# Kernel optimization log

Measured on AMD Instinct MI355X. Metric: run time of the kernel, lower is better.

## Reference

```python
import jax, jax.numpy as jnp
import numpy as np

N = 100000
E = 3200000
FEAT_DIMS = [512, 256, 128]
NUM_GNN = 2
NUM_MLP = 2
EPS = 1e-12


def l2norm(x):
    # F.normalize(x, dim=1, p=2)
    n = jnp.sqrt(jnp.sum(x * x, axis=1, keepdims=True))
    return x / jnp.maximum(n, EPS)


def setup_inputs() -> dict:
    key = jax.random.key(0)
    ks = jax.random.split(key, 16)
    D = FEAT_DIMS[-1]
    inp = {
        "feat": jax.random.normal(ks[0], (N, FEAT_DIMS[0]), dtype=jnp.float32),
        "sup_rows": jax.random.randint(ks[1], (E,), 0, N, dtype=jnp.int32),
        "sup_cols": jax.random.randint(ks[2], (E,), 0, N, dtype=jnp.int32),
        "sup_vals": jax.random.uniform(ks[3], (E,), dtype=jnp.float32),
        # feature-reduction linears (stored [in, out])
        "W_feat0": jax.random.normal(ks[4], (FEAT_DIMS[0], FEAT_DIMS[1]), dtype=jnp.float32) * 0.05,
        "b_feat0": jnp.zeros((FEAT_DIMS[1],), dtype=jnp.float32),
        "W_feat1": jax.random.normal(ks[5], (FEAT_DIMS[1], FEAT_DIMS[2]), dtype=jnp.float32) * 0.05,
        "b_feat1": jnp.zeros((FEAT_DIMS[2],), dtype=jnp.float32),
        # GCN layers (bias=False)
        "W_gnn": jax.random.normal(ks[6], (NUM_GNN, D, D), dtype=jnp.float32) * 0.05,
        # final emb linear map
        "W_emb": jax.random.normal(ks[7], (D, D), dtype=jnp.float32) * 0.05,
        "b_emb": jnp.zeros((D,), dtype=jnp.float32),
        # temperature MLP towers
        "W_lft": jax.random.normal(ks[8], (NUM_MLP, D, D), dtype=jnp.float32) * 0.05,
        "b_lft": jnp.zeros((NUM_MLP, D), dtype=jnp.float32),
        "W_rgt": jax.random.normal(ks[9], (NUM_MLP, D, D), dtype=jnp.float32) * 0.05,
        "b_rgt": jnp.zeros((NUM_MLP, D), dtype=jnp.float32),
    }
    return inp


def _forward(feat, sup_rows, sup_cols, sup_vals,
             W_feat0, b_feat0, W_feat1, b_feat1,
             W_gnn, W_emb, b_emb, W_lft, b_lft, W_rgt, b_rgt):
    # non-linear feature reduction (dropout = identity in eval mode)
    x = jnp.tanh(feat @ W_feat0 + b_feat0)
    x = jnp.tanh(x @ W_feat1 + b_feat1)

    def spmm(emb):
        # sparse support @ emb via gather + segment-sum
        msgs = sup_vals[:, None] * emb[sup_cols]           # [E, D]
        return jax.ops.segment_sum(msgs, sup_rows, num_segments=N)

    gnn_in = x
    gnn_acc = x
    gnn_out = x
    for l in range(NUM_GNN):
        h = spmm(gnn_in)
        h = jnp.tanh(h @ W_gnn[l])
        gnn_out = l2norm(h)
        gnn_in = gnn_out
        gnn_acc = gnn_acc + gnn_out

    emb = l2norm(gnn_acc @ W_emb + b_emb)

    lft_in = gnn_out
    rgt_in = gnn_out
    for l in range(NUM_MLP):
        lft = jnp.tanh(lft_in @ W_lft[l] + b_lft[l])
        rgt = jnp.tanh(rgt_in @ W_rgt[l] + b_rgt[l])
        if l < NUM_MLP - 1:
            lft = lft + lft_in
            rgt = rgt + rgt_in
        lft_in, rgt_in = lft, rgt
    return emb, lft_in, rgt_in


def reference(feat, sup_rows, sup_cols, sup_vals,
              W_feat0, b_feat0, W_feat1, b_feat1,
              W_gnn, W_emb, b_emb, W_lft, b_lft, W_rgt, b_rgt):
    return _forward(feat, sup_rows, sup_cols, sup_vals,
                    W_feat0, b_feat0, W_feat1, b_feat1,
                    W_gnn, W_emb, b_emb, W_lft, b_lft, W_rgt, b_rgt)
```

## Files before the change

kernel.cpp:

```cpp
#include <hip/hip_runtime.h>
#include <math.h>

typedef short bf16x8 __attribute__((ext_vector_type(8)));
typedef float f32x4  __attribute__((ext_vector_type(4)));

__device__ __forceinline__ unsigned short f2bf(float x) {
    unsigned u = __float_as_uint(x);
    unsigned r = u + 0x7FFFu + ((u >> 16) & 1u);
    return (unsigned short)(r >> 16);
}
__device__ __forceinline__ float bf2f(unsigned short b) {
    return __uint_as_float(((unsigned)b) << 16);
}

__global__ __launch_bounds__(256)
void wconvD(const float* __restrict__ W, unsigned short* __restrict__ Wt, int K, int N)
{
    int id = blockIdx.x * 256 + threadIdx.x;
    if (id >= K * N) return;
    int c = id / K, k = id - c * K;
    int kblk = k >> 5, ksub = (k >> 3) & 3, kel = k & 7;
    int cblk = c >> 6, n = c & 3, lr = (c >> 2) & 15;
    int lane = lr + (ksub << 4);
    size_t dst = ((((size_t)kblk * (N >> 6) + cblk) * 4 + n) << 9) + (lane << 3) + kel;
    Wt[dst] = f2bf(W[(size_t)k * N + c]);
}

__global__ __launch_bounds__(256)
void wconv7(const float* __restrict__ Wg, const float* __restrict__ Wemb,
            const float* __restrict__ Wl, const float* __restrict__ Wr,
            unsigned short* __restrict__ dst)
{
    int id = blockIdx.x * 256 + threadIdx.x;
    if (id >= 7 * 16384) return;
    int m = id >> 14, r = id & 16383;
    int c = r >> 7, k = r & 127;
    const float* src = (m < 2) ? (Wg + m * 16384)
                     : (m == 2) ? Wemb
                     : (m < 5) ? (Wl + (m - 3) * 16384)
                               : (Wr + (m - 5) * 16384);
    int n = c & 7, lr = (c >> 3) & 15;
    int ks = k >> 5, ksub = (k >> 3) & 3, kel = k & 7;
    int lane = lr + (ksub << 4);
    dst[(size_t)m * 16384 + (((ks << 3) + n) << 9) + (lane << 3) + kel] = f2bf(src[(size_t)k * 128 + c]);
}

__global__ __launch_bounds__(256)
void f32_to_bf16(const float* __restrict__ in, unsigned short* __restrict__ outb, long n8)
{
    long id = (long)blockIdx.x * 256 + threadIdx.x;
    if (id >= n8) return;
    const float4* p = (const float4*)(in + id * 8);
    float4 a = p[0], b = p[1];
    *(ushort4*)(outb + id * 8)     = make_ushort4(f2bf(a.x), f2bf(a.y), f2bf(a.z), f2bf(a.w));
    *(ushort4*)(outb + id * 8 + 4) = make_ushort4(f2bf(b.x), f2bf(b.y), f2bf(b.z), f2bf(b.w));
}

__global__ __launch_bounds__(512)
void mfma_head(const unsigned short* __restrict__ Ab, const unsigned short* __restrict__ Wt0,
               const float* __restrict__ bf0, const unsigned short* __restrict__ Wt1,
               const float* __restrict__ bf1, unsigned short* __restrict__ x_bf, int M)
{
    __shared__ __align__(16) unsigned short x1s[4][16][264];

    const int tid  = threadIdx.x;
    const int wv   = tid >> 6, lane = tid & 63;
    const int rg   = wv >> 1, ch = wv & 1;
    const int lr   = lane & 15;
    const int lk8  = (lane >> 4) * 8;
    const int rbase = (lane >> 4) * 4;
    const int row0 = blockIdx.x * 64 + rg * 16;

    const unsigned short* arow;
    { int r = row0 + lr; r = r < M ? r : (M - 1); arow = Ab + (size_t)r * 512 + lk8; }
    const unsigned short* bb0 = Wt0 + ((((size_t)ch * 2) * 4) << 9) + (lane << 3);

    f32x4 acc1[8];
#pragma unroll
    for (int s = 0; s < 8; s++)
#pragma unroll
        for (int q = 0; q < 4; q++) acc1[s][q] = 0.f;

#pragma unroll 2
    for (int kb = 0; kb < 16; kb++) {
        bf16x8 af = *(const bf16x8*)(arow + kb * 32);
        bf16x8 bn[8];
        const unsigned short* bk = bb0 + (((size_t)kb * 16) << 9);
#pragma unroll
        for (int s = 0; s < 8; s++) bn[s] = *(const bf16x8*)(bk + ((size_t)s << 9));
#pragma unroll
        for (int s = 0; s < 8; s++)
            acc1[s] = __builtin_amdgcn_mfma_f32_16x16x32_bf16(af, bn[s], acc1[s], 0, 0, 0);
    }

#pragma unroll
    for (int cb = 0; cb < 2; cb++) {
        int colp = (ch * 2 + cb) * 64 + lr * 4;
        float4 b4 = *(const float4*)(bf0 + colp);
        float bv[4] = {b4.x, b4.y, b4.z, b4.w};
#pragma unroll
        for (int j = 0; j < 4; j++) {
            ushort4 o;
            o.x = f2bf(tanhf(acc1[cb * 4 + 0][j] + bv[0]));
            o.y = f2bf(tanhf(acc1[cb * 4 + 1][j] + bv[1]));
            o.z = f2bf(tanhf(acc1[cb * 4 + 2][j] + bv[2]));
            o.w = f2bf(tanhf(acc1[cb * 4 + 3][j] + bv[3]));
            *(ushort4*)&x1s[rg][rbase + j][colp] = o;
        }
    }
    __syncthreads();

    const unsigned short* bb1 = Wt1 + ((((size_t)ch) * 4) << 9) + (lane << 3);

    f32x4 acc2[4];
#pragma unroll
    for (int n = 0; n < 4; n++)
#pragma unroll
        for (int q = 0; q < 4; q++) acc2[n][q] = 0.f;

#pragma unroll 2
    for (int ks = 0; ks < 8; ks++) {
        bf16x8 af = *(const bf16x8*)&x1s[rg][lr][ks * 32 + lk8];
        bf16x8 bn[4];
        const unsigned short* bk = bb1 + (((size_t)ks * 8) << 9);
#pragma unroll
        for (int n = 0; n < 4; n++) bn[n] = *(const bf16x8*)(bk + ((size_t)n << 9));
#pragma unroll
        for (int n = 0; n < 4; n++)
            acc2[n] = __builtin_amdgcn_mfma_f32_16x16x32_bf16(af, bn[n], acc2[n], 0, 0, 0);
    }

    const int cbase = ch * 64 + lr * 4;
    float4 b4 = *(const float4*)(bf1 + cbase);
    float bv[4] = {b4.x, b4.y, b4.z, b4.w};
#pragma unroll
    for (int j = 0; j < 4; j++) {
        int row = row0 + rbase + j;
        if (row < M) {
            ushort4 o;
            o.x = f2bf(tanhf(acc2[0][j] + bv[0]));
            o.y = f2bf(tanhf(acc2[1][j] + bv[1]));
            o.z = f2bf(tanhf(acc2[2][j] + bv[2]));
            o.w = f2bf(tanhf(acc2[3][j] + bv[3]));
            *(ushort4*)(x_bf + ((size_t)row << 7) + cbase) = o;
        }
    }
}

template<bool ABF16, bool TANH, bool L2, bool RESID, bool AUX, bool AUXBF,
         bool F32OUT, bool BF16OUT, bool BIAS>
__global__ __launch_bounds__(256)
void mfma_ep(const void* __restrict__ A_, const unsigned short* __restrict__ Wt,
             const float* __restrict__ bias, const unsigned short* __restrict__ resid_bf,
             const void* __restrict__ aux_in, float* __restrict__ aux_out,
             float* __restrict__ out, unsigned short* __restrict__ out_bf, int M)
{
    const int tid  = threadIdx.x;
    const int row0 = blockIdx.x * 64;
    const int wv   = tid >> 6, lane = tid & 63;
    const int lr   = lane & 15;
    const int lk8  = (lane >> 4) * 8;
    const int wr   = wv * 16;

    const unsigned short* Abr;
    const float*          Afr;
    {
        int r = row0 + wr + lr;
        r = r < M ? r : (M - 1);
        Abr = (const unsigned short*)A_ + ((size_t)r << 7) + lk8;
        Afr = (const float*)A_          + ((size_t)r << 7) + lk8;
    }
    const unsigned short* wb = Wt + (lane << 3);

    f32x4 acc[8];
#pragma unroll
    for (int n = 0; n < 8; n++)
#pragma unroll
        for (int j = 0; j < 4; j++) acc[n][j] = 0.f;

#pragma unroll 2
    for (int ks = 0; ks < 4; ks++) {
        bf16x8 af, bn[8];
        if (ABF16) af = *(const bf16x8*)(Abr + ks * 32);
        else {
            float4 a = *(const float4*)(Afr + ks * 32);
            float4 b = *(const float4*)(Afr + ks * 32 + 4);
            af[0]=(short)f2bf(a.x); af[1]=(short)f2bf(a.y); af[2]=(short)f2bf(a.z); af[3]=(short)f2bf(a.w);
            af[4]=(short)f2bf(b.x); af[5]=(short)f2bf(b.y); af[6]=(short)f2bf(b.z); af[7]=(short)f2bf(b.w);
        }
#pragma unroll
        for (int n = 0; n < 8; n++)
            bn[n] = *(const bf16x8*)(wb + ((((ks << 3) + n)) << 9));
#pragma unroll
        for (int n = 0; n < 8; n++)
            acc[n] = __builtin_amdgcn_mfma_f32_16x16x32_bf16(af, bn[n], acc[n], 0, 0, 0);
    }

    const int cbase = lr * 8;
    float bv[8];
    if (BIAS) {
        float4 b0 = *(const float4*)(bias + cbase);
        float4 b1 = *(const float4*)(bias + cbase + 4);
        bv[0]=b0.x; bv[1]=b0.y; bv[2]=b0.z; bv[3]=b0.w;
        bv[4]=b1.x; bv[5]=b1.y; bv[6]=b1.z; bv[7]=b1.w;
    } else {
#pragma unroll
        for (int n = 0; n < 8; n++) bv[n] = 0.f;
    }
    const int rbase = (lane >> 4) * 4;

#pragma unroll
    for (int j = 0; j < 4; j++) {
        int row = row0 + wr + rbase + j;
        bool ok = row < M;
        size_t base = ((size_t)row << 7) + cbase;
        float v[8];
#pragma unroll
        for (int n = 0; n < 8; n++) {
            v[n] = acc[n][j] + bv[n];
            if (TANH) v[n] = tanhf(v[n]);
        }
        if (RESID) {
            if (ok) {
                bf16x8 rv = *(const bf16x8*)(resid_bf + base);
#pragma unroll
                for (int n = 0; n < 8; n++) v[n] += bf2f((unsigned short)rv[n]);
            }
        }
        if (L2) {
            float s = 0.f;
#pragma unroll
            for (int n = 0; n < 8; n++) s += v[n] * v[n];
#pragma unroll
            for (int msk = 8; msk >= 1; msk >>= 1) s += __shfl_xor(s, msk);
            float sc = 1.f / fmaxf(sqrtf(s), 1e-12f);
#pragma unroll
            for (int n = 0; n < 8; n++) v[n] *= sc;
        }
        if (ok) {
            if (F32OUT) {
                *(float4*)(out + base)     = make_float4(v[0], v[1], v[2], v[3]);
                *(float4*)(out + base + 4) = make_float4(v[4], v[5], v[6], v[7]);
            }
            if (BF16OUT) {
                bf16x8 o;
#pragma unroll
                for (int n = 0; n < 8; n++) o[n] = (short)f2bf(v[n]);
                *(bf16x8*)(out_bf + base) = o;
            }
            if (AUX) {
                float ai[8];
                if (AUXBF) {
                    bf16x8 av = *(const bf16x8*)((const unsigned short*)aux_in + base);
#pragma unroll
                    for (int n = 0; n < 8; n++) ai[n] = bf2f((unsigned short)av[n]);
                } else {
                    float4 a0 = *(const float4*)((const float*)aux_in + base);
                    float4 a1 = *(const float4*)((const float*)aux_in + base + 4);
                    ai[0]=a0.x; ai[1]=a0.y; ai[2]=a0.z; ai[3]=a0.w;
                    ai[4]=a1.x; ai[5]=a1.y; ai[6]=a1.z; ai[7]=a1.w;
                }
                *(float4*)(aux_out + base)     = make_float4(ai[0]+v[0], ai[1]+v[1], ai[2]+v[2], ai[3]+v[3]);
                *(float4*)(aux_out + base + 4) = make_float4(ai[4]+v[4], ai[5]+v[5], ai[6]+v[6], ai[7]+v[7]);
            }
        }
    }
}

__global__ __launch_bounds__(256)
void tail_fused(const unsigned short* __restrict__ h_bf, const float* __restrict__ accf,
                const unsigned short* __restrict__ Wt7,
                const float* __restrict__ bemb, const float* __restrict__ bl,
                const float* __restrict__ br,
                float* __restrict__ embO, float* __restrict__ lftO,
                float* __restrict__ rgtO, int M)
{
    __shared__ __align__(16) unsigned short ldsA[4][16][136];
    __shared__ __align__(16) unsigned short ldsB[4][16][136];

    const int tid = threadIdx.x;
    const int wv = tid >> 6, lane = tid & 63;
    const int lr = lane & 15;
    const int lk8 = (lane >> 4) * 8;
    const int rbase = (lane >> 4) * 4;
    const int row0 = blockIdx.x * 64 + wv * 16;
    const int cbase = lr * 8;

    const unsigned short* Wg1t  = Wt7 + 1 * 16384 + (lane << 3);
    const unsigned short* Wembt = Wt7 + 2 * 16384 + (lane << 3);
    const unsigned short* Wl0t  = Wt7 + 3 * 16384 + (lane << 3);
    const unsigned short* Wl1t  = Wt7 + 4 * 16384 + (lane << 3);
    const unsigned short* Wr0t  = Wt7 + 5 * 16384 + (lane << 3);
    const unsigned short* Wr1t  = Wt7 + 6 * 16384 + (lane << 3);

    f32x4 acc[8];

#define ZACC() { _Pragma("unroll") for (int n = 0; n < 8; n++) \
                 _Pragma("unroll") for (int q = 0; q < 4; q++) acc[n][q] = 0.f; }
#define MM128(AFRAG, WPTR)                                                            \
    _Pragma("unroll")                                                                 \
    for (int ks = 0; ks < 4; ks++) {                                                  \
        bf16x8 af = (AFRAG);                                                          \
        bf16x8 bn[8];                                                                 \
        _Pragma("unroll")                                                             \
        for (int n = 0; n < 8; n++)                                                   \
            bn[n] = *(const bf16x8*)((WPTR) + ((((ks << 3) + n)) << 9));              \
        _Pragma("unroll")                                                             \
        for (int n = 0; n < 8; n++)                                                   \
            acc[n] = __builtin_amdgcn_mfma_f32_16x16x32_bf16(af, bn[n], acc[n], 0, 0, 0); \
    }
#define LDBIAS(BV, P) { float4 b0_ = *(const float4*)((P) + cbase);                   \
                        float4 b1_ = *(const float4*)((P) + cbase + 4);               \
                        BV[0]=b0_.x; BV[1]=b0_.y; BV[2]=b0_.z; BV[3]=b0_.w;           \
                        BV[4]=b1_.x; BV[5]=b1_.y; BV[6]=b1_.z; BV[7]=b1_.w; }
#define L2NORM(V) { float s_ = 0.f;                                                   \
                    _Pragma("unroll") for (int n = 0; n < 8; n++) s_ += V[n]*V[n];    \
                    _Pragma("unroll") for (int mk = 8; mk >= 1; mk >>= 1) s_ += __shfl_xor(s_, mk); \
                    float sc_ = 1.f / fmaxf(sqrtf(s_), 1e-12f);                       \
                    _Pragma("unroll") for (int n = 0; n < 8; n++) V[n] *= sc_; }

    const unsigned short* hrow;
    {
        int r = row0 + lr;
        r = r < M ? r : (M - 1);
        hrow = h_bf + ((size_t)r << 7) + lk8;
    }
    ZACC();
    MM128(*(const bf16x8*)(hrow + ks * 32), Wg1t);
#pragma unroll
    for (int j = 0; j < 4; j++) {
        int row = row0 + rbase + j;
        int rc = row < M ? row : (M - 1);
        float v[8];
#pragma unroll
        for (int n = 0; n < 8; n++) v[n] = tanhf(acc[n][j]);
        L2NORM(v);
        bf16x8 o;
#pragma unroll
        for (int n = 0; n < 8; n++) o[n] = (short)f2bf(v[n]);
        *(bf16x8*)&ldsA[wv][rbase + j][cbase] = o;
        float4 a0 = *(const float4*)(accf + ((size_t)rc << 7) + cbase);
        float4 a1 = *(const float4*)(accf + ((size_t)rc << 7) + cbase + 4);
        float av[8] = {a0.x+v[0], a0.y+v[1], a0.z+v[2], a0.w+v[3],
                       a1.x+v[4], a1.y+v[5], a1.z+v[6], a1.w+v[7]};
        bf16x8 ob;
#pragma unroll
        for (int n = 0; n < 8; n++) ob[n] = (short)f2bf(av[n]);
        *(bf16x8*)&ldsB[wv][rbase + j][cbase] = ob;
    }

    ZACC();
    MM128(*(const bf16x8*)&ldsB[wv][lr][ks * 32 + lk8], Wembt);
    {
        float bv[8]; LDBIAS(bv, bemb);
#pragma unroll
        for (int j = 0; j < 4; j++) {
            int row = row0 + rbase + j;
            float v[8];
#pragma unroll
            for (int n = 0; n < 8; n++) v[n] = acc[n][j] + bv[n];
            L2NORM(v);
            if (row < M) {
                size_t base = ((size_t)row << 7) + cbase;
                *(float4*)(embO + base)     = make_float4(v[0], v[1], v[2], v[3]);
                *(float4*)(embO + base + 4) = make_float4(v[4], v[5], v[6], v[7]);
            }
        }
    }

    ZACC();
    MM128(*(const bf16x8*)&ldsA[wv][lr][ks * 32 + lk8], Wl0t);
    {
        float bv[8]; LDBIAS(bv, bl);
#pragma unroll
        for (int j = 0; j < 4; j++) {
            bf16x8 rv = *(const bf16x8*)&ldsA[wv][rbase + j][cbase];
            bf16x8 ob;
#pragma unroll
            for (int n = 0; n < 8; n++)
                ob[n] = (short)f2bf(tanhf(acc[n][j] + bv[n]) + bf2f((unsigned short)rv[n]));
            *(bf16x8*)&ldsB[wv][rbase + j][cbase] = ob;
        }
    }

    ZACC();
    MM128(*(const bf16x8*)&ldsB[wv][lr][ks * 32 + lk8], Wl1t);
    {
        float bv[8]; LDBIAS(bv, bl + 128);
#pragma unroll
        for (int j = 0; j < 4; j++) {
            int row = row0 + rbase + j;
            if (row < M) {
                size_t base = ((size_t)row << 7) + cbase;
                *(float4*)(lftO + base)     = make_float4(tanhf(acc[0][j]+bv[0]), tanhf(acc[1][j]+bv[1]),
                                                          tanhf(acc[2][j]+bv[2]), tanhf(acc[3][j]+bv[3]));
                *(float4*)(lftO + base + 4) = make_float4(tanhf(acc[4][j]+bv[4]), tanhf(acc[5][j]+bv[5]),
                                                          tanhf(acc[6][j]+bv[6]), tanhf(acc[7][j]+bv[7]));
            }
        }
    }

    ZACC();
    MM128(*(const bf16x8*)&ldsA[wv][lr][ks * 32 + lk8], Wr0t);
    {
        float bv[8]; LDBIAS(bv, br);
#pragma unroll
        for (int j = 0; j < 4; j++) {
            bf16x8 rv = *(const bf16x8*)&ldsA[wv][rbase + j][cbase];
            bf16x8 ob;
#pragma unroll
            for (int n = 0; n < 8; n++)
                ob[n] = (short)f2bf(tanhf(acc[n][j] + bv[n]) + bf2f((unsigned short)rv[n]));
            *(bf16x8*)&ldsB[wv][rbase + j][cbase] = ob;
        }
    }

    ZACC();
    MM128(*(const bf16x8*)&ldsB[wv][lr][ks * 32 + lk8], Wr1t);
    {
        float bv[8]; LDBIAS(bv, br + 128);
#pragma unroll
        for (int j = 0; j < 4; j++) {
            int row = row0 + rbase + j;
            if (row < M) {
                size_t base = ((size_t)row << 7) + cbase;
                *(float4*)(rgtO + base)     = make_float4(tanhf(acc[0][j]+bv[0]), tanhf(acc[1][j]+bv[1]),
                                                          tanhf(acc[2][j]+bv[2]), tanhf(acc[3][j]+bv[3]));
                *(float4*)(rgtO + base + 4) = make_float4(tanhf(acc[4][j]+bv[4]), tanhf(acc[5][j]+bv[5]),
                                                          tanhf(acc[6][j]+bv[6]), tanhf(acc[7][j]+bv[7]));
            }
        }
    }
#undef ZACC
#undef MM128
#undef LDBIAS
#undef L2NORM
}

#define RCHUNK 16384

__global__ __launch_bounds__(256)
void bhist_k(const int* __restrict__ rows, int* __restrict__ bcnt, int E, int NB)
{
    __shared__ int lc[1024];
    for (int b = threadIdx.x; b < NB; b += 256) lc[b] = 0;
    __syncthreads();
    int start = blockIdx.x * RCHUNK;
    int end = min(start + RCHUNK, E);
    for (int i = start + threadIdx.x; i < end; i += 256)
        atomicAdd(&lc[rows[i] >> 7], 1);
    __syncthreads();
    for (int b = threadIdx.x; b < NB; b += 256)
        if (lc[b]) atomicAdd(&bcnt[b], lc[b]);
}

__global__ __launch_bounds__(256)
void bucket_scan(const int* __restrict__ bcnt, int* __restrict__ bbase,
                 int* __restrict__ bcur, int NB)
{
    __shared__ int sdata[256];
    const int tid = threadIdx.x;
    int loc[4]; int s = 0;
#pragma unroll
    for (int j = 0; j < 4; j++) {
        int i = tid * 4 + j;
        int v = (i < NB) ? bcnt[i] : 0;
        loc[j] = s; s += v;
    }
    sdata[tid] = s;
    __syncthreads();
    int x = s;
    for (int off = 1; off < 256; off <<= 1) {
        int t = 0;
        if (tid >= off) t = sdata[tid - off];
        __syncthreads();
        x += t;
        sdata[tid] = x;
        __syncthreads();
    }
    int excl = x - s;
#pragma unroll
    for (int j = 0; j < 4; j++) {
        int i = tid * 4 + j;
        if (i < NB) { bbase[i] = excl + loc[j]; bcur[i] = excl + loc[j]; }
    }
    if (tid == 255) bbase[NB] = x;
}

__global__ __launch_bounds__(256)
void bucket_scatter(const int* __restrict__ rows, const int* __restrict__ cols,
                    const float* __restrict__ vals, int* __restrict__ bcur,
                    int2* __restrict__ tmp, int E, int NB)
{
    __shared__ int lcnt[1024];
    __shared__ int lbase[1024];
    for (int b = threadIdx.x; b < NB; b += 256) lcnt[b] = 0;
    __syncthreads();
    int start = blockIdx.x * RCHUNK;
    int end = min(start + RCHUNK, E);
    for (int i = start + threadIdx.x; i < end; i += 256)
        atomicAdd(&lcnt[rows[i] >> 7], 1);
    __syncthreads();
    for (int b = threadIdx.x; b < NB; b += 256) {
        int c = lcnt[b];
        lbase[b] = c ? atomicAdd(&bcur[b], c) : 0;
        lcnt[b] = 0;
    }
    __syncthreads();
    for (int i = start + threadIdx.x; i < end; i += 256) {
        int r = rows[i];
        int b = r >> 7;
        int off = atomicAdd(&lcnt[b], 1);
        tmp[lbase[b] + off] = make_int2(cols[i] | ((r & 127) << 17), __float_as_int(vals[i]));
    }
}

__global__ __launch_bounds__(256)
void csr_place(const int2* __restrict__ tmp, const int* __restrict__ bbase,
               int* __restrict__ rowptr, int2* __restrict__ packed, int M, int NB)
{
    __shared__ int lcnt[128];
    __shared__ int lofs[128];
    const int tid = threadIdx.x;
    const int b = blockIdx.x;
    const int s = bbase[b], e = bbase[b + 1];
    const int rb = b << 7;
    if (tid < 128) lcnt[tid] = 0;
    __syncthreads();
    for (int i = s + tid; i < e; i += 256)
        atomicAdd(&lcnt[(((unsigned)tmp[i].x) >> 17) & 127], 1);
    __syncthreads();
    if (tid == 0) {
        int run = s;
#pragma unroll 8
        for (int r = 0; r < 128; r++) { lofs[r] = run; run += lcnt[r]; }
    }
    __syncthreads();
    if (tid < 128 && rb + tid < M) rowptr[rb + tid] = lofs[tid];
    if (b == NB - 1 && tid == 0) rowptr[M] = e;
    if (tid < 128) lcnt[tid] = 0;
    __syncthreads();
    for (int i = s + tid; i < e; i += 256) {
        int2 t = tmp[i];
        int rl = (((unsigned)t.x) >> 17) & 127;
        int pos = lofs[rl] + atomicAdd(&lcnt[rl], 1);
        packed[pos] = make_int2(t.x & 0x1FFFF, t.y);
    }
}

__global__ __launch_bounds__(256)
void spmm_csr(const int* __restrict__ rowptr, const int2* __restrict__ packed,
              const unsigned short* __restrict__ embb, unsigned short* __restrict__ hb, int N)
{
    const int wv = threadIdx.x >> 6, lane = threadIdx.x & 63;
    const int g = lane >> 4, q = lane & 15;
    const int r = blockIdx.x * 4 + wv;
    if (r >= N) return;
    const int s = rowptr[r], e = rowptr[r + 1];
    const unsigned short* __restrict__ eb = embb + q * 8;

    float a0=0.f,a1=0.f,a2=0.f,a3=0.f,a4=0.f,a5=0.f,a6=0.f,a7=0.f;
    int i = s + g;
    for (; i + 12 < e; i += 16) {
#pragma unroll
        for (int u = 0; u < 4; u++) {
            int2 p = packed[i + 4 * u];
            uint4 m = *(const uint4*)(eb + ((size_t)p.x << 7));
            float v = __int_as_float(p.y);
            a0 += v * __uint_as_float(m.x << 16);
            a1 += v * __uint_as_float(m.x & 0xffff0000u);
            a2 += v * __uint_as_float(m.y << 16);
            a3 += v * __uint_as_float(m.y & 0xffff0000u);
            a4 += v * __uint_as_float(m.z << 16);
            a5 += v * __uint_as_float(m.z & 0xffff0000u);
            a6 += v * __uint_as_float(m.w << 16);
            a7 += v * __uint_as_float(m.w & 0xffff0000u);
        }
    }
    for (; i < e; i += 4) {
        int2 p = packed[i];
        uint4 m = *(const uint4*)(eb + ((size_t)p.x << 7));
        float v = __int_as_float(p.y);
        a0 += v * __uint_as_float(m.x << 16);
        a1 += v * __uint_as_float(m.x & 0xffff0000u);
        a2 += v * __uint_as_float(m.y << 16);
        a3 += v * __uint_as_float(m.y & 0xffff0000u);
        a4 += v * __uint_as_float(m.z << 16);
        a5 += v * __uint_as_float(m.z & 0xffff0000u);
        a6 += v * __uint_as_float(m.w << 16);
        a7 += v * __uint_as_float(m.w & 0xffff0000u);
    }
#pragma unroll
    for (int msk = 16; msk <= 32; msk <<= 1) {
        a0 += __shfl_xor(a0, msk); a1 += __shfl_xor(a1, msk);
        a2 += __shfl_xor(a2, msk); a3 += __shfl_xor(a3, msk);
        a4 += __shfl_xor(a4, msk); a5 += __shfl_xor(a5, msk);
        a6 += __shfl_xor(a6, msk); a7 += __shfl_xor(a7, msk);
    }
    if (g == 0) {
        unsigned o0 = (unsigned)f2bf(a0) | ((unsigned)f2bf(a1) << 16);
        unsigned o1 = (unsigned)f2bf(a2) | ((unsigned)f2bf(a3) << 16);
        unsigned o2 = (unsigned)f2bf(a4) | ((unsigned)f2bf(a5) << 16);
        unsigned o3 = (unsigned)f2bf(a6) | ((unsigned)f2bf(a7) << 16);
        *(uint4*)(hb + ((size_t)r << 7) + q * 8) = make_uint4(o0, o1, o2, o3);
    }
}

extern "C" void kernel_launch(void* const* d_in, const int* in_sizes, int n_in,
                              void* d_out, int out_size, void* d_ws, size_t ws_size,
                              hipStream_t stream)
{
    const float* feat  = (const float*)d_in[0];
    const int*   srows = (const int*)  d_in[1];
    const int*   scols = (const int*)  d_in[2];
    const float* svals = (const float*)d_in[3];
    const float* Wf0   = (const float*)d_in[4];
    const float* bf0   = (const float*)d_in[5];
    const float* Wf1   = (const float*)d_in[6];
    const float* bf1   = (const float*)d_in[7];
    const float* Wg    = (const float*)d_in[8];
    const float* Wemb  = (const float*)d_in[9];
    const float* bemb  = (const float*)d_in[10];
    const float* Wl    = (const float*)d_in[11];
    const float* bl    = (const float*)d_in[12];
    const float* Wr    = (const float*)d_in[13];
    const float* br    = (const float*)d_in[14];

    const int M = in_sizes[0] / 512;
    const int E = in_sizes[1];
    const int NB = (M + 127) >> 7;

    float* out = (float*)d_out;
    float* R0 = out;
    float* R1 = out + (size_t)M * 128;
    float* R2 = out + (size_t)M * 256;

    float* ws = (float*)d_ws;
    float* accf = ws;
    int2*  tmp  = (int2*)ws;
    int*   ip = (int*)(ws + (size_t)M * 128);
    int*   rowptr  = ip;
    int2*  packed  = (int2*)(ip + (((size_t)M + 4) & ~(size_t)3));
    int*   bcnt    = (int*)(packed + E);
    int*   bbase   = bcnt + 1024;
    int*   bcur    = bbase + 1032;
    unsigned short* h_ws = (unsigned short*)(bcur + 1024);
    unsigned short* Wt0  = h_ws + (size_t)M * 128;
    unsigned short* Wt1  = Wt0 + 256 * 512;
    unsigned short* Wt7  = Wt1 + 128 * 256;

    unsigned short* R0a = (unsigned short*)R0;
    unsigned short* R1a = (unsigned short*)R1;
    unsigned short* feat_bf = (unsigned short*)R0;
    unsigned short* x_bf    = (unsigned short*)R2;
    unsigned short* n0_bf   = R1a;

    dim3 blk(256);
    const int gm64 = (M + 63) / 64;
    const int nch  = (E + RCHUNK - 1) / RCHUNK;

    wconvD<<<(512*256 + 255)/256, blk, 0, stream>>>(Wf0, Wt0, 512, 256);
    wconvD<<<(256*128 + 255)/256, blk, 0, stream>>>(Wf1, Wt1, 256, 128);
    wconv7<<<(7*16384 + 255)/256, blk, 0, stream>>>(Wg, Wemb, Wl, Wr, Wt7);

    f32_to_bf16<<<(int)(((long)M * 64 + 255) / 256), blk, 0, stream>>>(feat, feat_bf, (long)M * 64);

    hipMemsetAsync(bcnt, 0, (size_t)NB * 4, stream);
    bhist_k<<<nch, blk, 0, stream>>>(srows, bcnt, E, NB);
    bucket_scan<<<1, blk, 0, stream>>>(bcnt, bbase, bcur, NB);
    bucket_scatter<<<nch, blk, 0, stream>>>(srows, scols, svals, bcur, tmp, E, NB);
    csr_place<<<NB, blk, 0, stream>>>(tmp, bbase, rowptr, packed, M, NB);

    mfma_head<<<gm64, dim3(512), 0, stream>>>(feat_bf, Wt0, bf0, Wt1, bf1, x_bf, M);
    spmm_csr<<<(M + 3) / 4, blk, 0, stream>>>(rowptr, packed, x_bf, h_ws, M);
    mfma_ep<true,true,true,false,true,true,false,true,false><<<gm64,blk,0,stream>>>(
        h_ws, Wt7 , nullptr, nullptr, x_bf, accf, nullptr, n0_bf, M);
    spmm_csr<<<(M + 3) / 4, blk, 0, stream>>>(rowptr, packed, n0_bf, h_ws, M);
    tail_fused<<<gm64, blk, 0, stream>>>(h_ws, accf, Wt7, bemb, bl, br, R0, R1, R2, M);
}
```

Baseline: 729.6 us.

## Use exp-based fast tanh, raise unroll factors, add occupancy hints to launch bounds

Replaces every tanhf call with an __expf-based tanh approximation to cut transcendental cost in the GEMM epilogues. It also raises the unroll factor of the K loops in the feature-reduction kernel and adds a minimum-blocks-per-CU hint to the mfma_ep and tail_fused launch bounds. The fast tanh can overflow for large inputs (it stays correct through inf handling) and slightly changes accuracy. The launch-bound hint may cause register spills, and these epilogues are likely a small part of total time next to the sparse aggregation.

```diff
diff --git a/kernel.cpp b/kernel.cpp
--- a/kernel.cpp
+++ b/kernel.cpp
@@ -11,6 +11,10 @@
 }
 __device__ __forceinline__ float bf2f(unsigned short b) {
     return __uint_as_float(((unsigned)b) << 16);
+}
+__device__ __forceinline__ float fast_tanh(float x) {
+    float e = __expf(2.0f * x);
+    return 1.0f - 2.0f / (e + 1.0f);
 }
 
 __global__ __launch_bounds__(256)
@@ -81,7 +85,7 @@
 #pragma unroll
         for (int q = 0; q < 4; q++) acc1[s][q] = 0.f;
 
-#pragma unroll 2
+#pragma unroll 4
     for (int kb = 0; kb < 16; kb++) {
         bf16x8 af = *(const bf16x8*)(arow + kb * 32);
         bf16x8 bn[8];
@@ -101,10 +105,10 @@
 #pragma unroll
         for (int j = 0; j < 4; j++) {
             ushort4 o;
-            o.x = f2bf(tanhf(acc1[cb * 4 + 0][j] + bv[0]));
-            o.y = f2bf(tanhf(acc1[cb * 4 + 1][j] + bv[1]));
-            o.z = f2bf(tanhf(acc1[cb * 4 + 2][j] + bv[2]));
-            o.w = f2bf(tanhf(acc1[cb * 4 + 3][j] + bv[3]));
+            o.x = f2bf(fast_tanh(acc1[cb * 4 + 0][j] + bv[0]));
+            o.y = f2bf(fast_tanh(acc1[cb * 4 + 1][j] + bv[1]));
+            o.z = f2bf(fast_tanh(acc1[cb * 4 + 2][j] + bv[2]));
+            o.w = f2bf(fast_tanh(acc1[cb * 4 + 3][j] + bv[3]));
             *(ushort4*)&x1s[rg][rbase + j][colp] = o;
         }
     }
@@ -118,7 +122,7 @@
 #pragma unroll
         for (int q = 0; q < 4; q++) acc2[n][q] = 0.f;
 
-#pragma unroll 2
+#pragma unroll 4
     for (int ks = 0; ks < 8; ks++) {
         bf16x8 af = *(const bf16x8*)&x1s[rg][lr][ks * 32 + lk8];
         bf16x8 bn[4];
@@ -138,10 +142,10 @@
         int row = row0 + rbase + j;
         if (row < M) {
             ushort4 o;
-            o.x = f2bf(tanhf(acc2[0][j] + bv[0]));
-            o.y = f2bf(tanhf(acc2[1][j] + bv[1]));
-            o.z = f2bf(tanhf(acc2[2][j] + bv[2]));
-            o.w = f2bf(tanhf(acc2[3][j] + bv[3]));
+            o.x = f2bf(fast_tanh(acc2[0][j] + bv[0]));
+            o.y = f2bf(fast_tanh(acc2[1][j] + bv[1]));
+            o.z = f2bf(fast_tanh(acc2[2][j] + bv[2]));
+            o.w = f2bf(fast_tanh(acc2[3][j] + bv[3]));
             *(ushort4*)(x_bf + ((size_t)row << 7) + cbase) = o;
         }
     }
@@ -149,7 +153,7 @@
 
 template<bool ABF16, bool TANH, bool L2, bool RESID, bool AUX, bool AUXBF,
          bool F32OUT, bool BF16OUT, bool BIAS>
-__global__ __launch_bounds__(256)
+__global__ __launch_bounds__(256, 4)
 void mfma_ep(const void* __restrict__ A_, const unsigned short* __restrict__ Wt,
              const float* __restrict__ bias, const unsigned short* __restrict__ resid_bf,
              const void* __restrict__ aux_in, float* __restrict__ aux_out,
@@ -218,7 +222,7 @@
 #pragma unroll
         for (int n = 0; n < 8; n++) {
             v[n] = acc[n][j] + bv[n];
-            if (TANH) v[n] = tanhf(v[n]);
+            if (TANH) v[n] = fast_tanh(v[n]);
         }
         if (RESID) {
             if (ok) {
@@ -267,7 +271,7 @@
     }
 }
 
-__global__ __launch_bounds__(256)
+__global__ __launch_bounds__(256, 4)
 void tail_fused(const unsigned short* __restrict__ h_bf, const float* __restrict__ accf,
                 const unsigned short* __restrict__ Wt7,
                 const float* __restrict__ bemb, const float* __restrict__ bl,
@@ -333,7 +337,7 @@
         int rc = row < M ? row : (M - 1);
         float v[8];
 #pragma unroll
-        for (int n = 0; n < 8; n++) v[n] = tanhf(acc[n][j]);
+        for (int n = 0; n < 8; n++) v[n] = fast_tanh(acc[n][j]);
         L2NORM(v);
         bf16x8 o;
 #pragma unroll
@@ -378,7 +382,7 @@
             bf16x8 ob;
 #pragma unroll
             for (int n = 0; n < 8; n++)
-                ob[n] = (short)f2bf(tanhf(acc[n][j] + bv[n]) + bf2f((unsigned short)rv[n]));
+                ob[n] = (short)f2bf(fast_tanh(acc[n][j] + bv[n]) + bf2f((unsigned short)rv[n]));
             *(bf16x8*)&ldsB[wv][rbase + j][cbase] = ob;
         }
     }
@@ -392,10 +396,10 @@
             int row = row0 + rbase + j;
             if (row < M) {
                 size_t base = ((size_t)row << 7) + cbase;
-                *(float4*)(lftO + base)     = make_float4(tanhf(acc[0][j]+bv[0]), tanhf(acc[1][j]+bv[1]),
-                                                          tanhf(acc[2][j]+bv[2]), tanhf(acc[3][j]+bv[3]));
-                *(float4*)(lftO + base + 4) = make_float4(tanhf(acc[4][j]+bv[4]), tanhf(acc[5][j]+bv[5]),
-                                                          tanhf(acc[6][j]+bv[6]), tanhf(acc[7][j]+bv[7]));
+                *(float4*)(lftO + base)     = make_float4(fast_tanh(acc[0][j]+bv[0]), fast_tanh(acc[1][j]+bv[1]),
+                                                          fast_tanh(acc[2][j]+bv[2]), fast_tanh(acc[3][j]+bv[3]));
+                *(float4*)(lftO + base + 4) = make_float4(fast_tanh(acc[4][j]+bv[4]), fast_tanh(acc[5][j]+bv[5]),
+                                                          fast_tanh(acc[6][j]+bv[6]), fast_tanh(acc[7][j]+bv[7]));
             }
         }
     }
@@ -410,7 +414,7 @@
             bf16x8 ob;
 #pragma unroll
             for (int n = 0; n < 8; n++)
-                ob[n] = (short)f2bf(tanhf(acc[n][j] + bv[n]) + bf2f((unsigned short)rv[n]));
+                ob[n] = (short)f2bf(fast_tanh(acc[n][j] + bv[n]) + bf2f((unsigned short)rv[n]));
             *(bf16x8*)&ldsB[wv][rbase + j][cbase] = ob;
         }
     }
@@ -424,10 +428,10 @@
             int row = row0 + rbase + j;
             if (row < M) {
                 size_t base = ((size_t)row << 7) + cbase;
-                *(float4*)(rgtO + base)     = make_float4(tanhf(acc[0][j]+bv[0]), tanhf(acc[1][j]+bv[1]),
-                                                          tanhf(acc[2][j]+bv[2]), tanhf(acc[3][j]+bv[3]));
-                *(float4*)(rgtO + base + 4) = make_float4(tanhf(acc[4][j]+bv[4]), tanhf(acc[5][j]+bv[5]),
-                                                          tanhf(acc[6][j]+bv[6]), tanhf(acc[7][j]+bv[7]));
+                *(float4*)(rgtO + base)     = make_float4(fast_tanh(acc[0][j]+bv[0]), fast_tanh(acc[1][j]+bv[1]),
+                                                          fast_tanh(acc[2][j]+bv[2]), fast_tanh(acc[3][j]+bv[3]));
+                *(float4*)(rgtO + base + 4) = make_float4(fast_tanh(acc[4][j]+bv[4]), fast_tanh(acc[5][j]+bv[5]),
+                                                          fast_tanh(acc[6][j]+bv[6]), fast_tanh(acc[7][j]+bv[7]));
             }
         }
     }
@@ -649,7 +653,6 @@
     unsigned short* Wt1  = Wt0 + 256 * 512;
     unsigned short* Wt7  = Wt1 + 128 * 256;
 
-    unsigned short* R0a = (unsigned short*)R0;
     unsigned short* R1a = (unsigned short*)R1;
     unsigned short* feat_bf = (unsigned short*)R0;
     unsigned short* x_bf    = (unsigned short*)R2;
```

Measured after the change: 685.5 us. 1.06x faster.
